# Performance work log

Measured on AMD Instinct MI355X. Metric: run time of the kernel, lower is better.

## Reference

```python
import jax, jax.numpy as jnp
import numpy as np

B, S, D = 4, 2048, 2048


def setup_inputs() -> dict:
    key = jax.random.key(0)
    ks = jax.random.split(key, 9)
    scale = 1.0 / np.sqrt(D)
    x = jax.random.normal(ks[0], (B, S, D), dtype=jnp.float32)
    # causal mask, broadcast to [B, S, S]; 0 -> masked
    mask = jnp.broadcast_to(jnp.tril(jnp.ones((S, S), dtype=jnp.int32)), (B, S, S))
    Wq = jax.random.normal(ks[1], (D, D), dtype=jnp.float32) * scale
    Wk = jax.random.normal(ks[2], (D, D), dtype=jnp.float32) * scale
    Wv = jax.random.normal(ks[3], (D, D), dtype=jnp.float32) * scale
    Wp = jax.random.normal(ks[4], (D, D), dtype=jnp.float32) * scale
    bq = jnp.zeros((D,), jnp.float32)
    bk = jnp.zeros((D,), jnp.float32)
    bv = jnp.zeros((D,), jnp.float32)
    bp = jnp.zeros((D,), jnp.float32)
    return {"x": x, "mask": mask, "Wq": Wq, "bq": bq, "Wk": Wk, "bk": bk,
            "Wv": Wv, "bv": bv, "Wp": Wp, "bp": bp}


def reference(x, mask, Wq, bq, Wk, bk, Wv, bv, Wp, bp):
    # single-head scaled dot-product attention (cache=None path, eval mode)
    d_k = x.shape[-1]
    inv_std = 1.0 / jnp.sqrt(jnp.asarray(d_k, x.dtype))
    q = jnp.einsum('bsd,ed->bse', x, Wq) + bq  # nn.Linear: x @ W^T + b
    k = jnp.einsum('bsd,ed->bse', x, Wk) + bk
    v = jnp.einsum('bsd,ed->bse', x, Wv) + bv
    scores = jnp.einsum('bqd,bkd->bqk', q, k) * inv_std  # [B,S,S]
    scores = jnp.where(mask == 0, jnp.asarray(-jnp.inf, scores.dtype), scores)
    attn = jax.nn.softmax(scores, axis=-1)
    ctx = jnp.einsum('bqk,bkd->bqd', attn, v)
    out = jnp.einsum('bsd,ed->bse', ctx, Wp) + bp
    return out
```

## Files before the change

### kernel.cpp

```cpp
#include <hip/hip_runtime.h>
#include <hip/hip_bf16.h>
#include <type_traits>
#include <math.h>


typedef __bf16 bf16x8_t __attribute__((ext_vector_type(8)));
typedef float f32x4_t __attribute__((ext_vector_type(4)));
typedef unsigned short u16x8_t __attribute__((ext_vector_type(8)));

__device__ inline unsigned short f2bf(float f) {
  unsigned int u = __builtin_bit_cast(unsigned int, f);
  unsigned int r = u + 0x7fffu + ((u >> 16) & 1u);
  return (unsigned short)(r >> 16);
}

__device__ inline void gl2lds16(const unsigned short* g, unsigned short* l) {
  __builtin_amdgcn_global_load_lds(
      (const __attribute__((address_space(1))) unsigned int*)g,
      (__attribute__((address_space(3))) unsigned int*)l, 16, 0, 0);
}

__device__ __forceinline__ unsigned as3base(const unsigned short* p) {
  return (unsigned)(unsigned long long)
      (const __attribute__((address_space(3))) unsigned short*)p;
}

__device__ __forceinline__ bf16x8_t ldsa(unsigned a) {
  bf16x8_t r;
  asm volatile("ds_read_b128 %0, %1" : "=v"(r) : "v"(a));
  return r;
}

#define MF(a_, b_, c_) \
  (c_) = __builtin_amdgcn_mfma_f32_16x16x32_bf16((a_), (b_), (c_), 0, 0, 0)
#define SB0() __builtin_amdgcn_sched_barrier(0)
#define BAR()                         \
  do {                                \
    SB0();                            \
    __builtin_amdgcn_s_barrier();     \
    SB0();                            \
  } while (0)
#define LGK(n_)                                          \
  do {                                                   \
    asm volatile("s_waitcnt lgkmcnt(" #n_ ")");          \
    SB0();                                               \
  } while (0)
#define VM4()                                   \
  do {                                          \
    asm volatile("s_waitcnt vmcnt(4)");         \
    SB0();                                      \
  } while (0)
#define VM6()                                   \
  do {                                          \
    asm volatile("s_waitcnt vmcnt(6)");         \
    SB0();                                      \
  } while (0)
#define PRIO(x) __builtin_amdgcn_s_setprio(x)

__global__ __launch_bounds__(256) void cast_f32_bf16(
    const float* __restrict__ in, unsigned short* __restrict__ out, long n4) {
  long i = blockIdx.x * 256L + threadIdx.x;
  if (i >= n4) return;
  float4 f = ((const float4*)in)[i];
  ushort4 u;
  u.x = f2bf(f.x); u.y = f2bf(f.y); u.z = f2bf(f.z); u.w = f2bf(f.w);
  ((ushort4*)out)[i] = u;
}

__global__ __launch_bounds__(256) void cast_w4(
    const float* __restrict__ w0, const float* __restrict__ w1,
    const float* __restrict__ w2, const float* __restrict__ w3,
    unsigned short* __restrict__ o0, unsigned short* __restrict__ o1,
    unsigned short* __restrict__ o2, unsigned short* __restrict__ o3,
    long n4) {
  long i = blockIdx.x * 256L + threadIdx.x;
  if (i >= n4) return;
  const float* in; unsigned short* out;
  switch (blockIdx.y) {
    case 0: in = w0; out = o0; break;
    case 1: in = w1; out = o1; break;
    case 2: in = w2; out = o2; break;
    default: in = w3; out = o3; break;
  }
  float4 f = ((const float4*)in)[i];
  ushort4 u;
  u.x = f2bf(f.x); u.y = f2bf(f.y); u.z = f2bf(f.z); u.w = f2bf(f.w);
  ((ushort4*)out)[i] = u;
}

__device__ __forceinline__ void g256_kloop(
    const unsigned short* __restrict__ A, const unsigned short* __restrict__ B,
    int K, int Keff, unsigned short* smem, f32x4_t (&acc)[8][4]) {
  const int tid = threadIdx.x;
  const int lane = tid & 63;
  const int wave = tid >> 6;
  const int wr = wave >> 2;
  const int wc = wave & 3;
  const int fr = lane & 15;
  const int q4 = lane >> 4;
  const unsigned s0b = (unsigned)((q4 ^ (fr & 7)) * 16);
  const unsigned s1b = (unsigned)(((q4 + 4) ^ (fr & 7)) * 16);
  const size_t rowK =
      (size_t)(wave * 8 + (lane >> 3)) * (size_t)K +
      (size_t)(((lane & 7) ^ ((lane >> 3) & 7)) * 8);
  const size_t K64 = (size_t)64 * K;
  const size_t K128 = (size_t)128 * K;
  const int wofs = wave * 512;
  const int NT = Keff >> 6;
  const unsigned sb = as3base(smem);
  const unsigned aoffB = (unsigned)(wr * 16384 + fr * 128);
  const unsigned boffB =
      (unsigned)(32768 + (wc >> 1) * 16384 + (wc & 1) * 8192 + fr * 128);

#define STG(gp_, lh_)                        \
  do {                                       \
    const unsigned short* g_ = (gp_) + rowK; \
    gl2lds16(g_, (lh_) + wofs);              \
    gl2lds16(g_ + K64, (lh_) + 4096 + wofs); \
  } while (0)

#define MFMA8(mb_, af_)                          \
  _Pragma("unroll")                              \
  for (int n = 0; n < 4; ++n) {                  \
    MF(af_[0][0], bfr[n][0], acc[(mb_)][n]);     \
    MF(af_[0][1], bfr[n][1], acc[(mb_)][n]);     \
    MF(af_[1][0], bfr[n][0], acc[(mb_) + 1][n]); \
    MF(af_[1][1], bfr[n][1], acc[(mb_) + 1][n]); \
  }

#define RDA(dst_, baseB_, mo_)                                \
  _Pragma("unroll")                                           \
  for (int m = 0; m < 2; ++m) {                               \
    dst_[m][0] = ldsa((baseB_) + (m + (mo_)) * 2048u + s0b);  \
    dst_[m][1] = ldsa((baseB_) + (m + (mo_)) * 2048u + s1b);  \
  }

  STG(A, smem);
  STG(A + K128, smem + 8192);
  STG(B, smem + 16384);
  STG(B + K128, smem + 24576);
  STG(B + 64, smem + 32768 + 16384);
  STG(B + K128 + 64, smem + 32768 + 24576);
  STG(A + 64, smem + 32768);
  VM6();
  BAR();

  bf16x8_t bfr[4][2], a01[2][2], a23[2][2], a45[2][2], a67[2][2];
  {
    const unsigned Bh = sb + boffB;
    const unsigned Ah = sb + aoffB;
#pragma unroll
    for (int n = 0; n < 4; ++n) {
      bfr[n][0] = ldsa(Bh + n * 2048u + s0b);
      bfr[n][1] = ldsa(Bh + n * 2048u + s1b);
    }
    RDA(a01, Ah, 0);
  }

  for (int kt = 0; kt < NT; ++kt) {
    unsigned short* bcp = smem + ((kt & 1) << 15);
    unsigned short* nbp = smem + (((kt + 1) & 1) << 15);
    const unsigned AhcB = sb + ((unsigned)(kt & 1) << 16) + aoffB;
    const unsigned AhnB = sb + ((unsigned)((kt + 1) & 1) << 16) + aoffB;
    const unsigned BhnB = sb + ((unsigned)((kt + 1) & 1) << 16) + boffB;
    int k1 = (kt + 1) << 6; if (k1 >= Keff) k1 -= Keff;
    int k2 = (kt + 2) << 6; if (k2 >= Keff) k2 -= Keff;

    RDA(a23, AhcB, 2);
    SB0();
    STG(A + K128 + k1, nbp + 8192);
    BAR();
    LGK(4);
    PRIO(1);
    MFMA8(0, a01);
    PRIO(0);
    BAR();

    RDA(a45, AhcB, 4);
    SB0();
    STG(B + k2, bcp + 16384);
    BAR();
    LGK(4);
    PRIO(1);
    MFMA8(2, a23);
    PRIO(0);
    BAR();

    RDA(a67, AhcB, 6);
    SB0();
    STG(B + K128 + k2, bcp + 24576);
    BAR();
    LGK(4);
    PRIO(1);
    MFMA8(4, a45);
    PRIO(0);
    BAR();

    VM4();
    LGK(0);
    BAR();
    PRIO(1);
#pragma unroll
    for (int n = 0; n < 4; ++n) {
      MF(a67[0][0], bfr[n][0], acc[6][n]);
      MF(a67[0][1], bfr[n][1], acc[6][n]);
      MF(a67[1][0], bfr[n][0], acc[7][n]);
      MF(a67[1][1], bfr[n][1], acc[7][n]);
      bfr[n][0] = ldsa(BhnB + n * 2048u + s0b);
      bfr[n][1] = ldsa(BhnB + n * 2048u + s1b);
    }
    RDA(a01, AhnB, 0);
    PRIO(0);
    SB0();
    STG(A + k2, bcp);
    BAR();
  }
#undef STG
#undef MFMA8
#undef RDA
}

template <int MODE, typename OutT>
__global__ __launch_bounds__(512, 2) void gemm256_nt(
    const unsigned short* __restrict__ A, const unsigned short* __restrict__ B,
    OutT* __restrict__ C, const float* __restrict__ bias, float alpha,
    int N, int K, size_t sA, size_t sB, size_t sC) {
  int lin = blockIdx.y * gridDim.x + blockIdx.x;
  const int nwg = gridDim.x * gridDim.y;
  lin = (lin & 7) * (nwg >> 3) + (lin >> 3);
  const int bm = (lin / gridDim.x) * 256;
  const int bn = (lin % gridDim.x) * 256;
  if (MODE == 1 && bn >= bm + 256) return;
  int Keff = K;
  if (MODE == 2) { int kl = bm + 256; Keff = kl < K ? kl : K; }

  A += (size_t)blockIdx.z * sA + (size_t)bm * K;
  B += (size_t)blockIdx.z * sB + (size_t)bn * K;
  C += (size_t)blockIdx.z * sC;

  __shared__ unsigned short smem[65536];
  f32x4_t acc[8][4] = {};
  g256_kloop(A, B, K, Keff, smem, acc);

  const int tid = threadIdx.x;
  const int lane = tid & 63;
  const int wave = tid >> 6;
  const int wr = wave >> 2, wc = wave & 3;
  const int fr = lane & 15, q4 = lane >> 4;
  const int r0 = bm + wr * 128 + q4 * 4;
  const int c0 = bn + wc * 64 + fr;
#pragma unroll
  for (int n = 0; n < 4; ++n) {
    const int col = c0 + n * 16;
    const float bs = bias ? bias[col] : 0.f;
#pragma unroll
    for (int m = 0; m < 8; ++m) {
      const int row = r0 + m * 16;
#pragma unroll
      for (int r = 0; r < 4; ++r) {
        float v = acc[m][n][r] * alpha + bs;
        if constexpr (std::is_same_v<OutT, float>)
          C[(size_t)(row + r) * N + col] = v;
        else
          C[(size_t)(row + r) * N + col] = f2bf(v);
      }
    }
  }
}

__global__ __launch_bounds__(512, 2) void gemm256_qkv(
    const unsigned short* __restrict__ A, const unsigned short* __restrict__ Bw,
    unsigned short* __restrict__ Q, unsigned short* __restrict__ Kd,
    unsigned short* __restrict__ Vt,
    const float* __restrict__ bq, const float* __restrict__ bk,
    const float* __restrict__ bv, int K, int D, int S) {
  int lin = blockIdx.y * gridDim.x + blockIdx.x;
  const int nwg = gridDim.x * gridDim.y;
  lin = (lin & 7) * (nwg >> 3) + (lin >> 3);
  const int bm = (lin / gridDim.x) * 256;
  const int bn = (lin % gridDim.x) * 256;

  __shared__ unsigned short smem[65536];
  f32x4_t acc[8][4] = {};
  g256_kloop(A + (size_t)bm * K, Bw + (size_t)bn * K, K, K, smem, acc);

  const int tid = threadIdx.x;
  const int lane = tid & 63;
  const int wave = tid >> 6;
  const int wr = wave >> 2, wc = wave & 3;
  const int fr = lane & 15, q4 = lane >> 4;
  const int r0 = bm + wr * 128 + q4 * 4;
  const int c0 = bn + wc * 64 + fr;
#pragma unroll
  for (int n = 0; n < 4; ++n) {
    const int col = c0 + n * 16;
    const int sel = col >> 11;
    const int idx = col & (D - 1);
    const float bs = (sel == 0 ? bq : sel == 1 ? bk : bv)[idx];
#pragma unroll
    for (int m = 0; m < 8; ++m) {
      const int row = r0 + m * 16;
      if (sel < 2) {
        unsigned short* dst = sel == 0 ? Q : Kd;
#pragma unroll
        for (int r = 0; r < 4; ++r)
          dst[(size_t)(row + r) * D + idx] = f2bf(acc[m][n][r] + bs);
      } else {
        const int b = row >> 11;
        const int s = row & (S - 1);
        ushort4 pack;
        pack.x = f2bf(acc[m][n][0] + bs);
        pack.y = f2bf(acc[m][n][1] + bs);
        pack.z = f2bf(acc[m][n][2] + bs);
        pack.w = f2bf(acc[m][n][3] + bs);
        *(ushort4*)&Vt[(size_t)b * D * S + (size_t)idx * S + s] = pack;
      }
    }
  }
}

__global__ __launch_bounds__(256) void softmax_causal(
    const float* __restrict__ Sc, unsigned short* __restrict__ P, int n) {
  const int row = blockIdx.x;
  const int q = row & (n - 1);
  const float* srow = Sc + (size_t)row * n;
  unsigned short* prow = P + (size_t)row * n;
  const int tid = threadIdx.x, lane = tid & 63, wid = tid >> 6;
  __shared__ float red[4];

  float m = -3.0e38f;
  for (int j = tid; j <= q; j += 256) m = fmaxf(m, srow[j]);
#pragma unroll
  for (int o = 32; o; o >>= 1) m = fmaxf(m, __shfl_down(m, o, 64));
  if (lane == 0) red[wid] = m;
  __syncthreads();
  m = fmaxf(fmaxf(red[0], red[1]), fmaxf(red[2], red[3]));
  __syncthreads();

  float s = 0.f;
  for (int j = tid; j <= q; j += 256) s += __expf(srow[j] - m);
#pragma unroll
  for (int o = 32; o; o >>= 1) s += __shfl_down(s, o, 64);
  if (lane == 0) red[wid] = s;
  __syncthreads();
  s = red[0] + red[1] + red[2] + red[3];
  const float inv = 1.f / s;

  for (int j = tid; j < n; j += 256) {
    float v = (j <= q) ? __expf(srow[j] - m) * inv : 0.f;
    prow[j] = f2bf(v);
  }
}

extern "C" void kernel_launch(void* const* d_in, const int* in_sizes, int n_in,
                              void* d_out, int out_size, void* d_ws, size_t ws_size,
                              hipStream_t stream) {
  const int B = 4, S = 2048, D = 2048;
  const int M = B * S;

  const float* x  = (const float*)d_in[0];
  const float* Wq = (const float*)d_in[2];
  const float* bq = (const float*)d_in[3];
  const float* Wk = (const float*)d_in[4];
  const float* bk = (const float*)d_in[5];
  const float* Wv = (const float*)d_in[6];
  const float* bv = (const float*)d_in[7];
  const float* Wp = (const float*)d_in[8];
  const float* bp = (const float*)d_in[9];
  float* out = (float*)d_out;

  char* ws = (char*)d_ws;
  const size_t MB = 1ull << 20;
  unsigned short* xb   = (unsigned short*)(ws + 0);
  unsigned short* wqkv = (unsigned short*)(ws + 32 * MB);
  unsigned short* wpb  = (unsigned short*)(ws + 56 * MB);
  unsigned short* qb   = (unsigned short*)(ws + 64 * MB);
  unsigned short* kb   = (unsigned short*)(ws + 96 * MB);
  unsigned short* vtb  = (unsigned short*)(ws + 160 * MB);
  float*          sc   = (float*)(ws + 192 * MB);
  unsigned short* pb   = qb;
  unsigned short* cb   = kb;

  const long nx = (long)M * D;
  const long nw = (long)D * D;

  cast_f32_bf16<<<dim3((unsigned)((nx / 4 + 255) / 256)), 256, 0, stream>>>(x, xb, nx / 4);
  cast_w4<<<dim3((unsigned)((nw / 4 + 255) / 256), 4), 256, 0, stream>>>(
      Wq, Wk, Wv, Wp,
      wqkv, wqkv + (size_t)D * D, wqkv + 2 * (size_t)D * D, wpb, nw / 4);

  const dim3 blk(512);

  gemm256_qkv<<<dim3(3 * D / 256, M / 256), blk, 0, stream>>>(
      xb, wqkv, qb, kb, vtb, bq, bk, bv, D, D, S);

  const float inv_std = 1.f / sqrtf((float)D);
  gemm256_nt<1, float><<<dim3(S / 256, S / 256, B), blk, 0, stream>>>(
      qb, kb, sc, nullptr, inv_std, S, D, (size_t)S * D, (size_t)S * D, (size_t)S * S);

  softmax_causal<<<dim3(B * S), dim3(256), 0, stream>>>(sc, pb, S);

  gemm256_nt<2, unsigned short><<<dim3(D / 256, S / 256, B), blk, 0, stream>>>(
      pb, vtb, cb, nullptr, 1.f, D, S, (size_t)S * S, (size_t)D * S, (size_t)S * D);

  gemm256_nt<0, float><<<dim3(D / 256, M / 256), blk, 0, stream>>>(
      cb, wpb, out, bp, 1.f, D, D, 0, 0, 0);
}
```

Baseline: 620.9 us.

## Use 128x128 GEMM for attention matmuls and trim softmax padding writes

Adds a simpler 128x128-tile, 256-thread bf16 MFMA GEMM and uses it for the causal QK^T and P·V products. The finer tile granularity is meant to skip more masked work than the 256-tile kernel does. Softmax now writes zeros only up to the next 256-aligned column instead of the full row, cutting store traffic. Separately, the 256-tile k-loop now reads the first A fragment at the start of each iteration rather than prefetching it at the end of the previous one. The new kernel is single-buffered with two barriers per k-step, so it may reach lower throughput than the pipelined 256-tile kernel, and the moved A read removes some load/compute overlap in the projection GEMMs.

```diff
diff --git a/kernel.cpp b/kernel.cpp
--- a/kernel.cpp
+++ b/kernel.cpp
@@ -88,6 +88,112 @@
   ((ushort4*)out)[i] = u;
 }
 
+#define BM 128
+#define BN 128
+#define BK 64
+
+#define GEMM_PROLOGUE()                                                        \
+  const int tid = threadIdx.x;                                                 \
+  const int lane = tid & 63;                                                   \
+  const int wave = tid >> 6;                                                   \
+  const int wm = (wave >> 1) * 64;                                             \
+  const int wn = (wave & 1) * 64;                                              \
+  __shared__ unsigned short smem[2 * BM * BK];                      \
+  unsigned short* As = smem;                                                   \
+  unsigned short* Bs = smem + BM * BK;                                         \
+  const int lr = lane >> 3;                                                    \
+  const int swcol = ((lane & 7) ^ lr) * 8;                                     \
+  const int cbase = wave * 4;                                                  \
+  f32x4_t acc[4][4] = {};                                                      \
+  const int fr = lane & 15;                                                    \
+  const int q4 = lane >> 4;                                                    \
+  const int fo0 = ((q4 ^ (fr & 7)) * 8);             \
+  const int fo1 = (((q4 + 4) ^ (fr & 7)) * 8);
+
+#define GEMM_KLOOP(Ab, Bb, K, Keff)                                            \
+  for (int k0 = 0; k0 < (Keff); k0 += BK) {                                    \
+    __syncthreads();                                                           \
+    _Pragma("unroll")                                                          \
+    for (int i = 0; i < 4; i++) {                                              \
+      const int c = cbase + i;                                                 \
+      gl2lds16((Ab) + (size_t)(c * 8 + lr) * (K) + k0 + swcol, As + c * 512);  \
+      gl2lds16((Bb) + (size_t)(c * 8 + lr) * (K) + k0 + swcol, Bs + c * 512);  \
+    }                                                                          \
+    __syncthreads();                                                           \
+    {                                                                          \
+      bf16x8_t af[4], bfv[4];                                                  \
+      _Pragma("unroll")                                                        \
+      for (int mi = 0; mi < 4; mi++)                                           \
+        af[mi] = __builtin_bit_cast(                                           \
+            bf16x8_t, *(const u16x8_t*)&As[(wm + mi * 16 + fr) * BK + fo0]);   \
+      _Pragma("unroll")                                                        \
+      for (int ni = 0; ni < 4; ni++)                                           \
+        bfv[ni] = __builtin_bit_cast(                                          \
+            bf16x8_t, *(const u16x8_t*)&Bs[(wn + ni * 16 + fr) * BK + fo0]);   \
+      _Pragma("unroll")                                                        \
+      for (int mi = 0; mi < 4; mi++)                                           \
+        _Pragma("unroll")                                                      \
+        for (int ni = 0; ni < 4; ni++)                                         \
+          acc[mi][ni] = __builtin_amdgcn_mfma_f32_16x16x32_bf16(               \
+              af[mi], bfv[ni], acc[mi][ni], 0, 0, 0);                          \
+      _Pragma("unroll")                                                        \
+      for (int mi = 0; mi < 4; mi++)                                           \
+        af[mi] = __builtin_bit_cast(                                           \
+            bf16x8_t, *(const u16x8_t*)&As[(wm + mi * 16 + fr) * BK + fo1]);   \
+      _Pragma("unroll")                                                        \
+      for (int ni = 0; ni < 4; ni++)                                           \
+        bfv[ni] = __builtin_bit_cast(                                          \
+            bf16x8_t, *(const u16x8_t*)&Bs[(wn + ni * 16 + fr) * BK + fo1]);   \
+      _Pragma("unroll")                                                        \
+      for (int mi = 0; mi < 4; mi++)                                           \
+        _Pragma("unroll")                                                      \
+        for (int ni = 0; ni < 4; ni++)                                         \
+          acc[mi][ni] = __builtin_amdgcn_mfma_f32_16x16x32_bf16(               \
+              af[mi], bfv[ni], acc[mi][ni], 0, 0, 0);                          \
+    }                                                                          \
+  }
+
+template <int MODE, typename OutT>
+__global__ __launch_bounds__(256) void gemm128_nt(
+    const unsigned short* __restrict__ A, const unsigned short* __restrict__ B,
+    OutT* __restrict__ C, const float* __restrict__ bias, float alpha,
+    int M, int N, int K, size_t sA, size_t sB, size_t sC) {
+  const int bm = blockIdx.y * BM;
+  const int bn = blockIdx.x * BN;
+  if (MODE == 1 && bn >= bm + BM) return;
+  int Keff = K;
+  if (MODE == 2) { int kl = bm + BM; Keff = kl < K ? kl : K; }
+
+  A += (size_t)blockIdx.z * sA;
+  B += (size_t)blockIdx.z * sB;
+  C += (size_t)blockIdx.z * sC;
+
+  GEMM_PROLOGUE();
+  const unsigned short* Ab = A + (size_t)bm * K;
+  const unsigned short* Bb = B + (size_t)bn * K;
+  GEMM_KLOOP(Ab, Bb, K, Keff);
+
+  const int cr = (lane >> 4) * 4;
+  const int cc = lane & 15;
+#pragma unroll
+  for (int ni = 0; ni < 4; ni++) {
+    const int col = bn + wn + ni * 16 + cc;
+    const float bs = bias ? bias[col] : 0.f;
+#pragma unroll
+    for (int mi = 0; mi < 4; mi++) {
+      const int row = bm + wm + mi * 16 + cr;
+#pragma unroll
+      for (int r = 0; r < 4; r++) {
+        float v = acc[mi][ni][r] * alpha + bs;
+        if constexpr (std::is_same_v<OutT, float>)
+          C[(size_t)(row + r) * N + col] = v;
+        else
+          C[(size_t)(row + r) * N + col] = f2bf(v);
+      }
+    }
+  }
+}
+
 __device__ __forceinline__ void g256_kloop(
     const unsigned short* __restrict__ A, const unsigned short* __restrict__ B,
     int K, int Keff, unsigned short* smem, f32x4_t (&acc)[8][4]) {
@@ -148,24 +254,22 @@
   bf16x8_t bfr[4][2], a01[2][2], a23[2][2], a45[2][2], a67[2][2];
   {
     const unsigned Bh = sb + boffB;
-    const unsigned Ah = sb + aoffB;
 #pragma unroll
     for (int n = 0; n < 4; ++n) {
       bfr[n][0] = ldsa(Bh + n * 2048u + s0b);
       bfr[n][1] = ldsa(Bh + n * 2048u + s1b);
     }
-    RDA(a01, Ah, 0);
   }
 
   for (int kt = 0; kt < NT; ++kt) {
     unsigned short* bcp = smem + ((kt & 1) << 15);
     unsigned short* nbp = smem + (((kt + 1) & 1) << 15);
     const unsigned AhcB = sb + ((unsigned)(kt & 1) << 16) + aoffB;
-    const unsigned AhnB = sb + ((unsigned)((kt + 1) & 1) << 16) + aoffB;
     const unsigned BhnB = sb + ((unsigned)((kt + 1) & 1) << 16) + boffB;
     int k1 = (kt + 1) << 6; if (k1 >= Keff) k1 -= Keff;
     int k2 = (kt + 2) << 6; if (k2 >= Keff) k2 -= Keff;
 
+    RDA(a01, AhcB, 0);
     RDA(a23, AhcB, 2);
     SB0();
     STG(A + K128 + k1, nbp + 8192);
@@ -209,7 +313,6 @@
       bfr[n][0] = ldsa(BhnB + n * 2048u + s0b);
       bfr[n][1] = ldsa(BhnB + n * 2048u + s1b);
     }
-    RDA(a01, AhnB, 0);
     PRIO(0);
     SB0();
     STG(A + k2, bcp);
@@ -346,7 +449,8 @@
   s = red[0] + red[1] + red[2] + red[3];
   const float inv = 1.f / s;
 
-  for (int j = tid; j < n; j += 256) {
+  const int nwrite = ((q >> 8) + 1) << 8;
+  for (int j = tid; j < nwrite; j += 256) {
     float v = (j <= q) ? __expf(srow[j] - m) * inv : 0.f;
     prow[j] = f2bf(v);
   }
@@ -389,20 +493,18 @@
       Wq, Wk, Wv, Wp,
       wqkv, wqkv + (size_t)D * D, wqkv + 2 * (size_t)D * D, wpb, nw / 4);
 
-  const dim3 blk(512);
-
-  gemm256_qkv<<<dim3(3 * D / 256, M / 256), blk, 0, stream>>>(
+  gemm256_qkv<<<dim3(3 * D / 256, M / 256), dim3(512), 0, stream>>>(
       xb, wqkv, qb, kb, vtb, bq, bk, bv, D, D, S);
 
   const float inv_std = 1.f / sqrtf((float)D);
-  gemm256_nt<1, float><<<dim3(S / 256, S / 256, B), blk, 0, stream>>>(
-      qb, kb, sc, nullptr, inv_std, S, D, (size_t)S * D, (size_t)S * D, (size_t)S * S);
+  gemm128_nt<1, float><<<dim3(S / BN, S / BM, B), dim3(256), 0, stream>>>(
+      qb, kb, sc, nullptr, inv_std, S, S, D, (size_t)S * D, (size_t)S * D, (size_t)S * S);
 
   softmax_causal<<<dim3(B * S), dim3(256), 0, stream>>>(sc, pb, S);
 
-  gemm256_nt<2, unsigned short><<<dim3(D / 256, S / 256, B), blk, 0, stream>>>(
-      pb, vtb, cb, nullptr, 1.f, D, S, (size_t)S * S, (size_t)D * S, (size_t)S * D);
-
-  gemm256_nt<0, float><<<dim3(D / 256, M / 256), blk, 0, stream>>>(
+  gemm128_nt<2, unsigned short><<<dim3(D / BN, S / BM, B), dim3(256), 0, stream>>>(
+      pb, vtb, cb, nullptr, 1.f, S, D, S, (size_t)S * S, (size_t)D * S, (size_t)S * D);
+
+  gemm256_nt<0, float><<<dim3(D / 256, M / 256), dim3(512), 0, stream>>>(
       cb, wpb, out, bp, 1.f, D, D, 0, 0, 0);
 }
```

After: 654.1 us. +5.3%, slower.

## Restructure GEMM main loop into quadrant MFMA phases and trim softmax writes

Applied to the files above, without the earlier changes.

The 256x256 GEMM inner loop changes from eight A-row slices with the whole B fragment held in registers to four phases. Each phase multiplies a 4-row A fragment by a 2-column B fragment, and the global-to-LDS stages are regrouped and waited on with different vmcnt/lgkmcnt points. This cuts register pressure and B reloads per phase, but it drops the prefetch of next-tile fragments across iterations and adds full lgkmcnt(0) waits. The softmax kernel now writes bf16 probabilities only up to the 256-aligned column past the diagonal instead of the full row, skipping zero stores that the causal-aware PV GEMM (Keff limited) never reads.

```diff
diff --git a/kernel.cpp b/kernel.cpp
--- a/kernel.cpp
+++ b/kernel.cpp
@@ -44,11 +44,6 @@
   do {                                                   \
     asm volatile("s_waitcnt lgkmcnt(" #n_ ")");          \
     SB0();                                               \
-  } while (0)
-#define VM4()                                   \
-  do {                                          \
-    asm volatile("s_waitcnt vmcnt(4)");         \
-    SB0();                                      \
   } while (0)
 #define VM6()                                   \
   do {                                          \
@@ -119,21 +114,28 @@
     gl2lds16(g_ + K64, (lh_) + 4096 + wofs); \
   } while (0)
 
-#define MFMA8(mb_, af_)                          \
-  _Pragma("unroll")                              \
-  for (int n = 0; n < 4; ++n) {                  \
-    MF(af_[0][0], bfr[n][0], acc[(mb_)][n]);     \
-    MF(af_[0][1], bfr[n][1], acc[(mb_)][n]);     \
-    MF(af_[1][0], bfr[n][0], acc[(mb_) + 1][n]); \
-    MF(af_[1][1], bfr[n][1], acc[(mb_) + 1][n]); \
-  }
-
-#define RDA(dst_, baseB_, mo_)                                \
+#define RDAF(baseB_, mo_)                                     \
   _Pragma("unroll")                                           \
-  for (int m = 0; m < 2; ++m) {                               \
-    dst_[m][0] = ldsa((baseB_) + (m + (mo_)) * 2048u + s0b);  \
-    dst_[m][1] = ldsa((baseB_) + (m + (mo_)) * 2048u + s1b);  \
-  }
+  for (int m = 0; m < 4; ++m) {                               \
+    af[m][0] = ldsa((baseB_) + (m + (mo_)) * 2048u + s0b);    \
+    af[m][1] = ldsa((baseB_) + (m + (mo_)) * 2048u + s1b);    \
+  }
+
+#define RDB(dst_, baseB_, no_)                                \
+  _Pragma("unroll")                                           \
+  for (int n = 0; n < 2; ++n) {                               \
+    dst_[n][0] = ldsa((baseB_) + (n + (no_)) * 2048u + s0b);  \
+    dst_[n][1] = ldsa((baseB_) + (n + (no_)) * 2048u + s1b);  \
+  }
+
+#define MFQ(mb_, nb_, bsrc_)                                  \
+  _Pragma("unroll")                                           \
+  for (int m = 0; m < 4; ++m)                                 \
+    _Pragma("unroll")                                         \
+    for (int n = 0; n < 2; ++n) {                             \
+      MF(af[m][0], bsrc_[n][0], acc[(mb_) + m][(nb_) + n]);   \
+      MF(af[m][1], bsrc_[n][1], acc[(mb_) + m][(nb_) + n]);   \
+    }
 
   STG(A, smem);
   STG(A + K128, smem + 8192);
@@ -145,79 +147,60 @@
   VM6();
   BAR();
 
-  bf16x8_t bfr[4][2], a01[2][2], a23[2][2], a45[2][2], a67[2][2];
-  {
-    const unsigned Bh = sb + boffB;
-    const unsigned Ah = sb + aoffB;
-#pragma unroll
-    for (int n = 0; n < 4; ++n) {
-      bfr[n][0] = ldsa(Bh + n * 2048u + s0b);
-      bfr[n][1] = ldsa(Bh + n * 2048u + s1b);
-    }
-    RDA(a01, Ah, 0);
-  }
+  bf16x8_t af[4][2], bf0[2][2], bf1[2][2];
 
   for (int kt = 0; kt < NT; ++kt) {
     unsigned short* bcp = smem + ((kt & 1) << 15);
     unsigned short* nbp = smem + (((kt + 1) & 1) << 15);
     const unsigned AhcB = sb + ((unsigned)(kt & 1) << 16) + aoffB;
-    const unsigned AhnB = sb + ((unsigned)((kt + 1) & 1) << 16) + aoffB;
-    const unsigned BhnB = sb + ((unsigned)((kt + 1) & 1) << 16) + boffB;
+    const unsigned BhcB = sb + ((unsigned)(kt & 1) << 16) + boffB;
     int k1 = (kt + 1) << 6; if (k1 >= Keff) k1 -= Keff;
     int k2 = (kt + 2) << 6; if (k2 >= Keff) k2 -= Keff;
 
-    RDA(a23, AhcB, 2);
+    RDAF(AhcB, 0);
+    RDB(bf0, BhcB, 0);
     SB0();
     STG(A + K128 + k1, nbp + 8192);
-    BAR();
-    LGK(4);
+    LGK(8);
+    BAR();
+    LGK(0);
     PRIO(1);
-    MFMA8(0, a01);
+    MFQ(0, 0, bf0);
     PRIO(0);
     BAR();
 
-    RDA(a45, AhcB, 4);
+    RDB(bf1, BhcB, 2);
+    SB0();
+    BAR();
+    LGK(0);
+    PRIO(1);
+    MFQ(0, 2, bf1);
+    PRIO(0);
+    BAR();
+
+    RDAF(AhcB, 4);
     SB0();
     STG(B + k2, bcp + 16384);
-    BAR();
-    LGK(4);
+    STG(B + K128 + k2, bcp + 24576);
+    BAR();
+    LGK(0);
     PRIO(1);
-    MFMA8(2, a23);
+    MFQ(4, 0, bf0);
     PRIO(0);
     BAR();
 
-    RDA(a67, AhcB, 6);
-    SB0();
-    STG(B + K128 + k2, bcp + 24576);
-    BAR();
-    LGK(4);
+    STG(A + k2, bcp);
+    VM6();
+    BAR();
     PRIO(1);
-    MFMA8(4, a45);
+    MFQ(4, 2, bf1);
     PRIO(0);
     BAR();
-
-    VM4();
-    LGK(0);
-    BAR();
-    PRIO(1);
-#pragma unroll
-    for (int n = 0; n < 4; ++n) {
-      MF(a67[0][0], bfr[n][0], acc[6][n]);
-      MF(a67[0][1], bfr[n][1], acc[6][n]);
-      MF(a67[1][0], bfr[n][0], acc[7][n]);
-      MF(a67[1][1], bfr[n][1], acc[7][n]);
-      bfr[n][0] = ldsa(BhnB + n * 2048u + s0b);
-      bfr[n][1] = ldsa(BhnB + n * 2048u + s1b);
-    }
-    RDA(a01, AhnB, 0);
-    PRIO(0);
-    SB0();
-    STG(A + k2, bcp);
-    BAR();
   }
 #undef STG
-#undef MFMA8
-#undef RDA
+#undef RDAF
+#undef RDB
+#undef MFQ
 }
 
 template <int MODE, typename OutT>
@@ -346,7 +329,8 @@
   s = red[0] + red[1] + red[2] + red[3];
   const float inv = 1.f / s;
 
-  for (int j = tid; j < n; j += 256) {
+  const int nwrite = ((q >> 8) + 1) << 8;
+  for (int j = tid; j < nwrite; j += 256) {
     float v = (j <= q) ? __expf(srow[j] - m) * inv : 0.f;
     prow[j] = f2bf(v);
   }
```

Result: no change. 632.5 us (+1.9%).
